# Kernel optimization log

Measured on AMD Instinct MI355X. Metric: run time of the kernel, lower is better.

Reference implementation:

```python
import jax, jax.numpy as jnp
import numpy as np

B, N, D = 4, 8192, 128
H = 4 * D  # exp_factor * features
EPS = 1e-5


def layer_norm(x):
    # fresh nn.LayerNorm each call -> weight=1, bias=0 (no learned affine)
    mu = jnp.mean(x, axis=-1, keepdims=True)
    var = jnp.var(x, axis=-1, keepdims=True)
    return (x - mu) * jax.lax.rsqrt(var + EPS)


def setup_inputs() -> dict:
    key = jax.random.key(0)
    ks = jax.random.split(key, 8)
    x = jax.random.normal(ks[0], (B, N, D), dtype=jnp.float32)
    adj = jax.random.uniform(ks[1], (N, N), dtype=jnp.float32)
    attn_mask = jnp.ones((1,), dtype=jnp.int32)  # unused (torch masked_fill result discarded)
    pad_mask = jnp.ones((1,), dtype=jnp.int32)   # unused
    # FFN params (torch Linear default init scale ~ 1/sqrt(fan_in))
    w1 = jax.random.normal(ks[2], (D, H), dtype=jnp.float32) / np.sqrt(D)
    b1 = jnp.zeros((H,), dtype=jnp.float32)
    w2 = jax.random.normal(ks[3], (H, D), dtype=jnp.float32) / np.sqrt(H)
    b2 = jnp.zeros((D,), dtype=jnp.float32)
    return {"x": x, "adj": adj, "attn_mask": attn_mask, "pad_mask": pad_mask,
            "w1": w1, "b1": b1, "w2": w2, "b2": b2, "dim": 128}


def reference(x, adj, attn_mask, pad_mask, w1, b1, w2, b2, dim):
    # Sublayer 0: x + InrAwaSA(LN(x))
    h = layer_norm(x)                               # [B,N,D]
    # adj is provided -> scores = dense adj, shared across batch.
    # NOTE: masks are no-ops in the source (masked_fill not in-place).
    prob = jax.nn.softmax(adj, axis=-1)             # [N,N]
    attn_out = jnp.einsum('nm,bmd->bnd', prob, h)   # [B,N,D]
    x1 = x + attn_out
    # Sublayer 1: x1 + FFN(LN(x1))
    h1 = layer_norm(x1)
    ffn = jnp.maximum(h1 @ w1 + b1, 0.0) @ w2 + b2
    return x1 + ffn
```

## Files before the change

kernel.cpp:

```cpp
#include <hip/hip_runtime.h>
#include <hip/hip_bf16.h>

typedef __attribute__((ext_vector_type(8))) short bh8;
typedef __attribute__((ext_vector_type(4))) float fx4;
typedef __attribute__((ext_vector_type(8))) int i32x8;
typedef __attribute__((ext_vector_type(4))) int i32x4;

typedef const __attribute__((address_space(1))) unsigned int* gas_p;
typedef __attribute__((address_space(3))) unsigned int* las_p;

#define MFMA(a, b, c) __builtin_amdgcn_mfma_f32_16x16x32_bf16((a), (b), (c), 0, 0, 0)
#define MFMAS(a, b, c) __builtin_amdgcn_mfma_scale_f32_16x16x128_f8f6f4( \
    (a), (b), (c), 0, 0, 0, 0x7f7f7f7f, 0, 0x7f7f7f7f)

__device__ __forceinline__ unsigned short f2bf(float f) {
  unsigned u = __builtin_bit_cast(unsigned, f);
  u += 0x7fff + ((u >> 16) & 1);
  return (unsigned short)(u >> 16);
}

__device__ __forceinline__ float bflo2f(unsigned u) { return __builtin_bit_cast(float, u << 16); }

__device__ __forceinline__ void gld16(const void* g, void* l) {
  __builtin_amdgcn_global_load_lds((gas_p)g, (las_p)l, 16, 0, 0);
}

__global__ __launch_bounds__(256) void transpose_weights(const float* __restrict__ w1,
                                                         const float* __restrict__ w2,
                                                         unsigned short* __restrict__ w1t,
                                                         unsigned short* __restrict__ w2t) {
  const int tgl = blockIdx.x * 256 + threadIdx.x;
  { const int h = tgl >> 7, d = tgl & 127; w1t[tgl] = f2bf(w1[d * 512 + h]); }
  { const int d = tgl >> 9, h = tgl & 511; w2t[tgl] = f2bf(w2[h * 128 + d]); }
}

__global__ __launch_bounds__(256) void ln1_transpose(const float* __restrict__ x,
                                                     unsigned char* __restrict__ ht) {
  const int t = threadIdx.x, lane = t & 63, w = t >> 6;
  const int mt = blockIdx.x, b = blockIdx.y;
  __shared__ unsigned short tile[128 * 64];
  const float* xb = x + ((size_t)b * 8192 + (size_t)mt * 64) * 128;
  for (int it = 0; it < 16; ++it) {
    const int r = w * 16 + it;
    const float2 v = *(const float2*)(xb + r * 128 + lane * 2);
    float s = v.x + v.y, s2 = v.x * v.x + v.y * v.y;
    #pragma unroll
    for (int o = 1; o < 64; o <<= 1) { s += __shfl_xor(s, o); s2 += __shfl_xor(s2, o); }
    const float mean = s * 0.0078125f;
    const float var = s2 * 0.0078125f - mean * mean;
    const float rstd = rsqrtf(var + 1e-5f);
    const int mc = r >> 3, ml = r & 7;
    const int d0 = lane * 2, d1 = d0 + 1;
    tile[d0 * 64 + ((mc ^ (d0 & 7)) << 3) + ml] = f2bf((v.x - mean) * rstd);
    tile[d1 * 64 + ((mc ^ (d1 & 7)) << 3) + ml] = f2bf((v.y - mean) * rstd);
  }
  __syncthreads();
  unsigned char* hb = ht + (size_t)b * 128 * 8192 + (size_t)mt * 64;
  #pragma unroll
  for (int i = 0; i < 4; ++i) {
    const int idx = i * 256 + t;
    const int d = idx >> 3, mc = idx & 7;
    const bh8 vv = *(const bh8*)(tile + d * 64 + ((mc ^ (d & 7)) << 3));
    int lo = 0, hi = 0;
    lo = __builtin_amdgcn_cvt_pk_fp8_f32(bflo2f((unsigned short)vv[0]),
                                         bflo2f((unsigned short)vv[1]), lo, false);
    lo = __builtin_amdgcn_cvt_pk_fp8_f32(bflo2f((unsigned short)vv[2]),
                                         bflo2f((unsigned short)vv[3]), lo, true);
    hi = __builtin_amdgcn_cvt_pk_fp8_f32(bflo2f((unsigned short)vv[4]),
                                         bflo2f((unsigned short)vv[5]), hi, false);
    hi = __builtin_amdgcn_cvt_pk_fp8_f32(bflo2f((unsigned short)vv[6]),
                                         bflo2f((unsigned short)vv[7]), hi, true);
    *(uint2*)(hb + (size_t)d * 8192 + mc * 8) = (uint2){(unsigned)lo, (unsigned)hi};
  }
}

__global__ __launch_bounds__(256) void softmax_rows(const float* __restrict__ adj,
                                                    unsigned char* __restrict__ prob) {
  const int t = threadIdx.x, lane = t & 63, w = t >> 6;
  const size_t r = blockIdx.x;
  __shared__ float red[4];
  const fx4* row = (const fx4*)(adj + r * 8192);
  fx4 v[8];
  float lsum = 0.f;
  #pragma unroll
  for (int i = 0; i < 8; ++i) {
    const fx4 a = row[i * 256 + t];
    fx4 e;
    e.x = __expf(a.x);
    e.y = __expf(a.y);
    e.z = __expf(a.z);
    e.w = __expf(a.w);
    v[i] = e;
    lsum += e.x + e.y + e.z + e.w;
  }
  #pragma unroll
  for (int o = 1; o < 64; o <<= 1) lsum += __shfl_xor(lsum, o);
  if (lane == 0) red[w] = lsum;
  __syncthreads();
  const float rinv = 4096.f / (red[0] + red[1] + red[2] + red[3]);
  unsigned* po = (unsigned*)(prob + r * 8192);
  #pragma unroll
  for (int i = 0; i < 8; ++i) {
    int pk = 0;
    pk = __builtin_amdgcn_cvt_pk_fp8_f32(v[i].x * rinv, v[i].y * rinv, pk, false);
    pk = __builtin_amdgcn_cvt_pk_fp8_f32(v[i].z * rinv, v[i].w * rinv, pk, true);
    po[i * 256 + t] = (unsigned)pk;
  }
}

#define PH_SYNC { __builtin_amdgcn_sched_barrier(0); __builtin_amdgcn_s_barrier(); \
                  __builtin_amdgcn_sched_barrier(0); \
                  asm volatile("s_waitcnt lgkmcnt(0)" ::: "memory"); \
                  __builtin_amdgcn_sched_barrier(0); __builtin_amdgcn_s_setprio(1); }
#define PH_END  { __builtin_amdgcn_s_setprio(0); __builtin_amdgcn_sched_barrier(0); \
                  __builtin_amdgcn_s_barrier(); __builtin_amdgcn_sched_barrier(0); }
#define PH_END_VM4 { __builtin_amdgcn_s_setprio(0); \
                  asm volatile("s_waitcnt vmcnt(4)" ::: "memory"); \
                  __builtin_amdgcn_sched_barrier(0); __builtin_amdgcn_s_barrier(); \
                  __builtin_amdgcn_sched_barrier(0); }

__global__ __launch_bounds__(512, 2) void attn_gemm(const unsigned char* __restrict__ prob,
                                                    const unsigned char* __restrict__ ht,
                                                    unsigned short* __restrict__ pbuf) {
  const int t = threadIdx.x, lane = t & 63, w = t >> 6;
  const int wm = w >> 2, wn = w & 3;
  const int mt = blockIdx.x, nt = blockIdx.y, z = blockIdx.z;
  const int kbase = z * 2048;

  __shared__ unsigned char Al[2][2][128 * 128];
  __shared__ unsigned char Bl[2][2][128 * 128];

  fx4 acc[8][4];
  #pragma unroll
  for (int i = 0; i < 8; ++i)
    #pragma unroll
    for (int j = 0; j < 4; ++j) acc[i][j] = (fx4){0.f, 0.f, 0.f, 0.f};

  i32x8 afr[4], bf0[2], bf1[2];

  auto stageA = [&](int buf, int half, int tau) {
    const unsigned char* root = prob + (size_t)(mt * 256 + half * 128) * 8192 + kbase + tau * 128;
    #pragma unroll
    for (int j = 0; j < 2; ++j) {
      const int idx = j * 512 + t;
      const int r = idx >> 3, g = idx & 7;
      gld16(root + (size_t)r * 8192 + ((g ^ (r & 7)) << 4), &Al[buf][half][idx * 16]);
    }
  };
  auto stageB = [&](int buf, int half, int tau) {
    const unsigned char* root = ht + (size_t)(nt * 256 + half * 128) * 8192 + kbase + tau * 128;
    #pragma unroll
    for (int j = 0; j < 2; ++j) {
      const int idx = j * 512 + t;
      const int r = idx >> 3, g = idx & 7;
      gld16(root + (size_t)r * 8192 + ((g ^ (r & 7)) << 4), &Bl[buf][half][idx * 16]);
    }
  };
  auto ldA = [&](int buf, int mh) {
    #pragma unroll
    for (int mf = 0; mf < 4; ++mf) {
      const int r = mh * 64 + mf * 16 + (lane & 15);
      const int gb = (lane >> 4) * 2;
      const unsigned char* base = &Al[buf][wm][r * 128];
      const i32x4 lo = *(const i32x4*)(base + ((gb ^ (r & 7)) << 4));
      const i32x4 hi = *(const i32x4*)(base + (((gb + 1) ^ (r & 7)) << 4));
      afr[mf] = (i32x8){lo.x, lo.y, lo.z, lo.w, hi.x, hi.y, hi.z, hi.w};
    }
  };
  auto ldB = [&](int buf, int nh, i32x8* dst) {
    #pragma unroll
    for (int nf = 0; nf < 2; ++nf) {
      const int c = (wn & 1) * 64 + nh * 32 + nf * 16 + (lane & 15);
      const int gb = (lane >> 4) * 2;
      const unsigned char* base = &Bl[buf][wn >> 1][c * 128];
      const i32x4 lo = *(const i32x4*)(base + ((gb ^ (c & 7)) << 4));
      const i32x4 hi = *(const i32x4*)(base + (((gb + 1) ^ (c & 7)) << 4));
      dst[nf] = (i32x8){lo.x, lo.y, lo.z, lo.w, hi.x, hi.y, hi.z, hi.w};
    }
  };
  auto mmq = [&](int mh, int nh, const i32x8* bfr) {
    #pragma unroll
    for (int mf = 0; mf < 4; ++mf)
      #pragma unroll
      for (int nf = 0; nf < 2; ++nf)
        acc[mh * 4 + mf][nh * 2 + nf] = MFMAS(afr[mf], bfr[nf], acc[mh * 4 + mf][nh * 2 + nf]);
  };

  stageA(0, 0, 0); stageA(0, 1, 0); stageB(0, 0, 0); stageB(0, 1, 0);
  stageB(1, 0, 1); stageB(1, 1, 1);
  asm volatile("s_waitcnt vmcnt(4)" ::: "memory");
  __builtin_amdgcn_sched_barrier(0);
  __builtin_amdgcn_s_barrier();
  __builtin_amdgcn_sched_barrier(0);

  for (int i = 0; i < 7; ++i) {
    const int t0 = 2 * i;
    ldA(0, 0); ldB(0, 0, bf0); stageA(1, 0, t0 + 1);
    PH_SYNC; mmq(0, 0, bf0); PH_END;
    ldB(0, 1, bf1); stageA(1, 1, t0 + 1);
    PH_SYNC; mmq(0, 1, bf1); PH_END;
    ldA(0, 1); stageB(0, 0, t0 + 2);
    PH_SYNC; mmq(1, 1, bf1); PH_END;
    stageB(0, 1, t0 + 2);
    PH_SYNC; mmq(1, 0, bf0); PH_END_VM4;
    ldA(1, 0); ldB(1, 0, bf0); stageA(0, 0, t0 + 2);
    PH_SYNC; mmq(0, 0, bf0); PH_END;
    ldB(1, 1, bf1); stageA(0, 1, t0 + 2);
    PH_SYNC; mmq(0, 1, bf1); PH_END;
    ldA(1, 1); stageB(1, 0, t0 + 3);
    PH_SYNC; mmq(1, 1, bf1); PH_END;
    stageB(1, 1, t0 + 3);
    PH_SYNC; mmq(1, 0, bf0); PH_END_VM4;
  }

  stageA(1, 0, 15); stageA(1, 1, 15);
  asm volatile("s_waitcnt vmcnt(0)" ::: "memory");
  __builtin_amdgcn_sched_barrier(0);
  __builtin_amdgcn_s_barrier();
  __builtin_amdgcn_sched_barrier(0);
  ldA(0, 0); ldB(0, 0, bf0); PH_SYNC; mmq(0, 0, bf0); PH_END;
  ldB(0, 1, bf1);            PH_SYNC; mmq(0, 1, bf1); PH_END;
  ldA(0, 1);                 PH_SYNC; mmq(1, 1, bf1); PH_END;
                             PH_SYNC; mmq(1, 0, bf0); PH_END;
  ldA(1, 0); ldB(1, 0, bf0); PH_SYNC; mmq(0, 0, bf0); PH_END;
  ldB(1, 1, bf1);            PH_SYNC; mmq(0, 1, bf1); PH_END;
  ldA(1, 1);                 PH_SYNC; mmq(1, 1, bf1); PH_END;
                             PH_SYNC; mmq(1, 0, bf0); PH_END;

  const float ds = 0.000244140625f;
  unsigned short* po = pbuf + (size_t)z * 8192 * 512;
  const int grow0 = mt * 256 + wm * 128;
  const int gcol0 = nt * 256 + (wn >> 1) * 128 + (wn & 1) * 64;
  #pragma unroll
  for (int mh = 0; mh < 2; ++mh)
    #pragma unroll
    for (int mf = 0; mf < 4; ++mf)
      #pragma unroll
      for (int nh = 0; nh < 2; ++nh)
        #pragma unroll
        for (int nf = 0; nf < 2; ++nf) {
          const int col = gcol0 + nh * 32 + nf * 16 + (lane & 15);
          #pragma unroll
          for (int q = 0; q < 4; ++q) {
            const int row = grow0 + mh * 64 + mf * 16 + (lane >> 4) * 4 + q;
            po[(size_t)row * 512 + col] = f2bf(acc[mh * 4 + mf][nh * 2 + nf][q] * ds);
          }
        }
}

#define SWZ16(ks, r) (((((ks) & 7) ^ ((r) & 7)) | ((ks) & 8)))
__global__ __launch_bounds__(512) void ln_ffn_kernel(const float* __restrict__ x,
                                                     const unsigned short* __restrict__ pbuf,
                                                     const unsigned short* __restrict__ w1t,
                                                     const unsigned short* __restrict__ w2t,
                                                     const float* __restrict__ b1,
                                                     const float* __restrict__ b2,
                                                     float* __restrict__ out) {
  const int t = threadIdx.x, lane = t & 63, w = t >> 6;
  const int wr = w >> 1, wc = w & 1;
  const int row0 = blockIdx.x * 128;
  __shared__ unsigned short As[128 * 128];
  __shared__ unsigned short W1c[128 * 128];
  __shared__ unsigned short W2c[128 * 128];
  __shared__ unsigned short Ts[128 * 128];

  auto stageW1 = [&](int hc) {
    #pragma unroll
    for (int i = 0; i < 4; ++i) {
      const int idx = i * 512 + t;
      const int row = idx >> 4, kc = idx & 15;
      const int kcs = (kc & 8) | ((kc & 7) ^ (row & 7));
      gld16(w1t + (size_t)(hc * 128 + row) * 128 + kcs * 8, W1c + (idx & ~63) * 8);
    }
  };
  auto stageW2 = [&](int hc) {
    #pragma unroll
    for (int i = 0; i < 4; ++i) {
      const int idx = i * 512 + t;
      const int row = idx >> 4, kc = idx & 15;
      const int kcs = (kc & 8) | ((kc & 7) ^ (row & 7));
      gld16(w2t + (size_t)row * 512 + hc * 128 + kcs * 8, W2c + (idx & ~63) * 8);
    }
  };

  stageW1(0); stageW2(0);

  const int r = t >> 2, q = t & 3, c0 = q * 32;
  const int rowg = row0 + r;
  const int bb = rowg >> 13, nn = rowg & 8191;
  float xv[32];
  {
    const float* xp = x + (size_t)rowg * 128 + c0;
    #pragma unroll
    for (int j = 0; j < 8; ++j) {
      const float4 v4 = *(const float4*)(xp + 4 * j);
      xv[4 * j] = v4.x; xv[4 * j + 1] = v4.y; xv[4 * j + 2] = v4.z; xv[4 * j + 3] = v4.w;
    }
    #pragma unroll
    for (int z = 0; z < 4; ++z) {
      const unsigned short* pp = pbuf + ((size_t)z * 8192 + nn) * 512 + bb * 128 + c0;
      #pragma unroll
      for (int j = 0; j < 4; ++j) {
        const bh8 pv = *(const bh8*)(pp + 8 * j);
        #pragma unroll
        for (int e = 0; e < 8; ++e) xv[8 * j + e] += bflo2f((unsigned short)pv[e]);
      }
    }
  }
  float s = 0.f, s2 = 0.f;
  #pragma unroll
  for (int j = 0; j < 32; ++j) { s += xv[j]; s2 += xv[j] * xv[j]; }
  s += __shfl_xor(s, 1); s2 += __shfl_xor(s2, 1);
  s += __shfl_xor(s, 2); s2 += __shfl_xor(s2, 2);
  const float mean = s * 0.0078125f;
  const float var = s2 * 0.0078125f - mean * mean;
  const float rstd = rsqrtf(var + 1e-5f);
  #pragma unroll
  for (int j = 0; j < 4; ++j) {
    const int g = q * 4 + j;
    bh8 pk;
    #pragma unroll
    for (int e = 0; e < 8; ++e) pk[e] = (short)f2bf((xv[8 * j + e] - mean) * rstd);
    *(bh8*)(As + r * 128 + SWZ16(g, r) * 8) = pk;
  }
  __syncthreads();

  fx4 accO[2][4];
  #pragma unroll
  for (int i = 0; i < 2; ++i)
    #pragma unroll
    for (int j = 0; j < 4; ++j) accO[i][j] = (fx4){0.f, 0.f, 0.f, 0.f};

  for (int hc = 0; hc < 4; ++hc) {
    if (hc > 0) stageW2(hc);
    fx4 accT[2][4];
    #pragma unroll
    for (int i = 0; i < 2; ++i)
      #pragma unroll
      for (int j = 0; j < 4; ++j) accT[i][j] = (fx4){0.f, 0.f, 0.f, 0.f};
    #pragma unroll
    for (int kk = 0; kk < 4; ++kk) {
      const int ks = kk * 4 + (lane >> 4);
      bh8 af[2], bfr[4];
      #pragma unroll
      for (int f = 0; f < 2; ++f) {
        const int ra = wr * 32 + f * 16 + (lane & 15);
        af[f] = *(const bh8*)(As + ra * 128 + SWZ16(ks, ra) * 8);
      }
      #pragma unroll
      for (int f = 0; f < 4; ++f) {
        const int rb = wc * 64 + f * 16 + (lane & 15);
        bfr[f] = *(const bh8*)(W1c + rb * 128 + SWZ16(ks, rb) * 8);
      }
      #pragma unroll
      for (int fm = 0; fm < 2; ++fm)
        #pragma unroll
        for (int fn = 0; fn < 4; ++fn) accT[fm][fn] = MFMA(af[fm], bfr[fn], accT[fm][fn]);
    }
    #pragma unroll
    for (int fm = 0; fm < 2; ++fm)
      #pragma unroll
      for (int fn = 0; fn < 4; ++fn) {
        const int col = wc * 64 + fn * 16 + (lane & 15);
        const float bv = b1[hc * 128 + col];
        const int c = col >> 3;
        #pragma unroll
        for (int qq = 0; qq < 4; ++qq) {
          const int row = wr * 32 + fm * 16 + (lane >> 4) * 4 + qq;
          float vv = accT[fm][fn][qq] + bv;
          vv = fmaxf(vv, 0.f);
          Ts[row * 128 + SWZ16(c, row) * 8 + (col & 7)] = f2bf(vv);
        }
      }
    __syncthreads();
    if (hc < 3) {
      stageW1(hc + 1);
    } else {
      float* dst = (r < 64) ? (float*)As + r * 128 + c0 : (float*)W1c + (r - 64) * 128 + c0;
      #pragma unroll
      for (int j = 0; j < 8; ++j)
        *(float4*)(dst + 4 * j) =
            (float4){xv[4 * j], xv[4 * j + 1], xv[4 * j + 2], xv[4 * j + 3]};
    }
    #pragma unroll
    for (int kk = 0; kk < 4; ++kk) {
      const int ks = kk * 4 + (lane >> 4);
      bh8 af[2], bfr[4];
      #pragma unroll
      for (int f = 0; f < 2; ++f) {
        const int ra = wr * 32 + f * 16 + (lane & 15);
        af[f] = *(const bh8*)(Ts + ra * 128 + SWZ16(ks, ra) * 8);
      }
      #pragma unroll
      for (int f = 0; f < 4; ++f) {
        const int rb = wc * 64 + f * 16 + (lane & 15);
        bfr[f] = *(const bh8*)(W2c + rb * 128 + SWZ16(ks, rb) * 8);
      }
      #pragma unroll
      for (int fm = 0; fm < 2; ++fm)
        #pragma unroll
        for (int fn = 0; fn < 4; ++fn) accO[fm][fn] = MFMA(af[fm], bfr[fn], accO[fm][fn]);
    }
    __syncthreads();
  }

  const float* x1a = (const float*)As;
  const float* x1b = (const float*)W1c;
  float* op = out + (size_t)row0 * 128;
  #pragma unroll
  for (int fm = 0; fm < 2; ++fm)
    #pragma unroll
    for (int fn = 0; fn < 4; ++fn) {
      const int col = wc * 64 + fn * 16 + (lane & 15);
      const float bv = b2[col];
      #pragma unroll
      for (int qq = 0; qq < 4; ++qq) {
        const int row = wr * 32 + fm * 16 + (lane >> 4) * 4 + qq;
        const float x1v = (row < 64) ? x1a[row * 128 + col] : x1b[(row - 64) * 128 + col];
        op[row * 128 + col] = x1v + accO[fm][fn][qq] + bv;
      }
    }
}

extern "C" void kernel_launch(void* const* d_in, const int* in_sizes, int n_in,
                              void* d_out, int out_size, void* d_ws, size_t ws_size,
                              hipStream_t stream) {
  const float* x   = (const float*)d_in[0];
  const float* adj = (const float*)d_in[1];
  const float* w1  = (const float*)d_in[4];
  const float* b1  = (const float*)d_in[5];
  const float* w2  = (const float*)d_in[6];
  const float* b2  = (const float*)d_in[7];
  float* out = (float*)d_out;

  char* p = (char*)d_ws;
  unsigned short* w1t  = (unsigned short*)p; p += (size_t)512 * 128 * 2;
  unsigned short* w2t  = (unsigned short*)p; p += (size_t)128 * 512 * 2;
  unsigned char*  ht   = (unsigned char*)p;  p += (size_t)4 * 128 * 8192;
  unsigned short* pbuf = (unsigned short*)p; p += (size_t)4 * 8192 * 512 * 2;
  unsigned char*  prob = (unsigned char*)p;  p += (size_t)8192 * 8192;

  transpose_weights<<<256, 256, 0, stream>>>(w1, w2, w1t, w2t);
  ln1_transpose<<<dim3(128, 4), 256, 0, stream>>>(x, ht);
  softmax_rows<<<8192, 256, 0, stream>>>(adj, prob);
  attn_gemm<<<dim3(32, 2, 4), 512, 0, stream>>>(prob, ht, pbuf);
  ln_ffn_kernel<<<256, 512, 0, stream>>>(x, pbuf, w1t, w2t, b1, b2, out);
}
```

Baseline: 157.6 us.

## Fuse softmax exponentiation into attention GEMM and defer normalization to LN-FFN

Removes the separate softmax kernel and its 64 MB fp8 probability buffer. The attention GEMM now reads fp32 adj directly, computes exp and converts to fp8 in registers, writes the A tile to LDS, and accumulates per-row partial denominators that are stored per K-split. The LN/FFN kernel sums the four partial denominators and scales the attention output by their reciprocal. The tile shape changes to 128 rows by all 512 columns with double-buffered B, so each block reads adj once. In exchange each block does exp work inside the GEMM loop, waits on vmcnt(0) each step, and stores unscaled exp values in fp8, which may reduce precision.

```diff
diff --git a/kernel.cpp b/kernel.cpp
--- a/kernel.cpp
+++ b/kernel.cpp
@@ -74,183 +74,142 @@
   }
 }
 
-__global__ __launch_bounds__(256) void softmax_rows(const float* __restrict__ adj,
-                                                    unsigned char* __restrict__ prob) {
-  const int t = threadIdx.x, lane = t & 63, w = t >> 6;
-  const size_t r = blockIdx.x;
-  __shared__ float red[4];
-  const fx4* row = (const fx4*)(adj + r * 8192);
-  fx4 v[8];
-  float lsum = 0.f;
-  #pragma unroll
-  for (int i = 0; i < 8; ++i) {
-    const fx4 a = row[i * 256 + t];
-    fx4 e;
-    e.x = __expf(a.x);
-    e.y = __expf(a.y);
-    e.z = __expf(a.z);
-    e.w = __expf(a.w);
-    v[i] = e;
-    lsum += e.x + e.y + e.z + e.w;
-  }
-  #pragma unroll
-  for (int o = 1; o < 64; o <<= 1) lsum += __shfl_xor(lsum, o);
-  if (lane == 0) red[w] = lsum;
-  __syncthreads();
-  const float rinv = 4096.f / (red[0] + red[1] + red[2] + red[3]);
-  unsigned* po = (unsigned*)(prob + r * 8192);
-  #pragma unroll
-  for (int i = 0; i < 8; ++i) {
-    int pk = 0;
-    pk = __builtin_amdgcn_cvt_pk_fp8_f32(v[i].x * rinv, v[i].y * rinv, pk, false);
-    pk = __builtin_amdgcn_cvt_pk_fp8_f32(v[i].z * rinv, v[i].w * rinv, pk, true);
-    po[i * 256 + t] = (unsigned)pk;
-  }
-}
-
 #define PH_SYNC { __builtin_amdgcn_sched_barrier(0); __builtin_amdgcn_s_barrier(); \
                   __builtin_amdgcn_sched_barrier(0); \
                   asm volatile("s_waitcnt lgkmcnt(0)" ::: "memory"); \
                   __builtin_amdgcn_sched_barrier(0); __builtin_amdgcn_s_setprio(1); }
 #define PH_END  { __builtin_amdgcn_s_setprio(0); __builtin_amdgcn_sched_barrier(0); \
                   __builtin_amdgcn_s_barrier(); __builtin_amdgcn_sched_barrier(0); }
-#define PH_END_VM4 { __builtin_amdgcn_s_setprio(0); \
-                  asm volatile("s_waitcnt vmcnt(4)" ::: "memory"); \
+#define PH_END_VM0 { __builtin_amdgcn_s_setprio(0); \
+                  asm volatile("s_waitcnt vmcnt(0)" ::: "memory"); \
                   __builtin_amdgcn_sched_barrier(0); __builtin_amdgcn_s_barrier(); \
                   __builtin_amdgcn_sched_barrier(0); }
 
-__global__ __launch_bounds__(512, 2) void attn_gemm(const unsigned char* __restrict__ prob,
-                                                    const unsigned char* __restrict__ ht,
-                                                    unsigned short* __restrict__ pbuf) {
-  const int t = threadIdx.x, lane = t & 63, w = t >> 6;
+__global__ __launch_bounds__(512, 2) void fused_attn(const float* __restrict__ adj,
+                                                     const unsigned char* __restrict__ ht,
+                                                     unsigned short* __restrict__ pbuf,
+                                                     float* __restrict__ sden) {
+  const int tid = threadIdx.x, lane = tid & 63, w = tid >> 6;
   const int wm = w >> 2, wn = w & 3;
-  const int mt = blockIdx.x, nt = blockIdx.y, z = blockIdx.z;
+  const int mt = blockIdx.x, z = blockIdx.y;
   const int kbase = z * 2048;
 
-  __shared__ unsigned char Al[2][2][128 * 128];
-  __shared__ unsigned char Bl[2][2][128 * 128];
-
-  fx4 acc[8][4];
-  #pragma unroll
-  for (int i = 0; i < 8; ++i)
-    #pragma unroll
-    for (int j = 0; j < 4; ++j) acc[i][j] = (fx4){0.f, 0.f, 0.f, 0.f};
-
-  i32x8 afr[4], bf0[2], bf1[2];
-
-  auto stageA = [&](int buf, int half, int tau) {
-    const unsigned char* root = prob + (size_t)(mt * 256 + half * 128) * 8192 + kbase + tau * 128;
-    #pragma unroll
-    for (int j = 0; j < 2; ++j) {
-      const int idx = j * 512 + t;
-      const int r = idx >> 3, g = idx & 7;
-      gld16(root + (size_t)r * 8192 + ((g ^ (r & 7)) << 4), &Al[buf][half][idx * 16]);
-    }
-  };
-  auto stageB = [&](int buf, int half, int tau) {
-    const unsigned char* root = ht + (size_t)(nt * 256 + half * 128) * 8192 + kbase + tau * 128;
-    #pragma unroll
-    for (int j = 0; j < 2; ++j) {
-      const int idx = j * 512 + t;
-      const int r = idx >> 3, g = idx & 7;
-      gld16(root + (size_t)r * 8192 + ((g ^ (r & 7)) << 4), &Bl[buf][half][idx * 16]);
-    }
-  };
-  auto ldA = [&](int buf, int mh) {
+  __shared__ unsigned char Al[128 * 128];
+  __shared__ unsigned char Bl[2][512 * 128];
+
+  fx4 acc[4][8];
+  #pragma unroll
+  for (int i = 0; i < 4; ++i)
+    #pragma unroll
+    for (int j = 0; j < 8; ++j) acc[i][j] = (fx4){0.f, 0.f, 0.f, 0.f};
+
+  i32x8 afr[4];
+
+  const int ar = tid >> 2, aq = tid & 3;
+  const float* aroot = adj + (size_t)(mt * 128 + ar) * 8192 + kbase;
+  float sacc = 0.f;
+  float4 a4[8];
+  unsigned pk[8];
+
+  auto issueAdj = [&](int tau) {
+    #pragma unroll
+    for (int j = 0; j < 8; ++j)
+      a4[j] = *(const float4*)(aroot + tau * 128 + j * 16 + aq * 4);
+  };
+  auto expCvt = [&]() {
+    #pragma unroll
+    for (int j = 0; j < 8; ++j) {
+      const float e0 = __expf(a4[j].x), e1 = __expf(a4[j].y);
+      const float e2 = __expf(a4[j].z), e3 = __expf(a4[j].w);
+      sacc += (e0 + e1) + (e2 + e3);
+      int d = 0;
+      d = __builtin_amdgcn_cvt_pk_fp8_f32(e0, e1, d, false);
+      d = __builtin_amdgcn_cvt_pk_fp8_f32(e2, e3, d, true);
+      pk[j] = (unsigned)d;
+    }
+  };
+  auto writeA = [&]() {
+    #pragma unroll
+    for (int j = 0; j < 8; ++j)
+      *(unsigned*)&Al[ar * 128 + ((j ^ (ar & 7)) << 4) + aq * 4] = pk[j];
+  };
+  auto stageB2 = [&](unsigned char* dst, int pp, int tau) {
+    #pragma unroll
+    for (int k = 0; k < 2; ++k) {
+      const int cc = pp * 2 + k;
+      const int row = cc * 64 + (tid >> 3), g = tid & 7;
+      gld16(ht + (size_t)row * 8192 + kbase + tau * 128 + ((g ^ (row & 7)) << 4),
+            dst + cc * 8192 + tid * 16);
+    }
+  };
+  auto ldAall = [&]() {
     #pragma unroll
     for (int mf = 0; mf < 4; ++mf) {
-      const int r = mh * 64 + mf * 16 + (lane & 15);
+      const int rr = wm * 64 + mf * 16 + (lane & 15);
       const int gb = (lane >> 4) * 2;
-      const unsigned char* base = &Al[buf][wm][r * 128];
-      const i32x4 lo = *(const i32x4*)(base + ((gb ^ (r & 7)) << 4));
-      const i32x4 hi = *(const i32x4*)(base + (((gb + 1) ^ (r & 7)) << 4));
+      const unsigned char* base = &Al[rr * 128];
+      const i32x4 lo = *(const i32x4*)(base + ((gb ^ (rr & 7)) << 4));
+      const i32x4 hi = *(const i32x4*)(base + (((gb + 1) ^ (rr & 7)) << 4));
       afr[mf] = (i32x8){lo.x, lo.y, lo.z, lo.w, hi.x, hi.y, hi.z, hi.w};
     }
   };
-  auto ldB = [&](int buf, int nh, i32x8* dst) {
-    #pragma unroll
-    for (int nf = 0; nf < 2; ++nf) {
-      const int c = (wn & 1) * 64 + nh * 32 + nf * 16 + (lane & 15);
-      const int gb = (lane >> 4) * 2;
-      const unsigned char* base = &Bl[buf][wn >> 1][c * 128];
-      const i32x4 lo = *(const i32x4*)(base + ((gb ^ (c & 7)) << 4));
-      const i32x4 hi = *(const i32x4*)(base + (((gb + 1) ^ (c & 7)) << 4));
-      dst[nf] = (i32x8){lo.x, lo.y, lo.z, lo.w, hi.x, hi.y, hi.z, hi.w};
-    }
-  };
-  auto mmq = [&](int mh, int nh, const i32x8* bfr) {
-    #pragma unroll
-    for (int mf = 0; mf < 4; ++mf)
-      #pragma unroll
-      for (int nf = 0; nf < 2; ++nf)
-        acc[mh * 4 + mf][nh * 2 + nf] = MFMAS(afr[mf], bfr[nf], acc[mh * 4 + mf][nh * 2 + nf]);
-  };
-
-  stageA(0, 0, 0); stageA(0, 1, 0); stageB(0, 0, 0); stageB(0, 1, 0);
-  stageB(1, 0, 1); stageB(1, 1, 1);
-  asm volatile("s_waitcnt vmcnt(4)" ::: "memory");
+
+  issueAdj(0);
+  #pragma unroll
+  for (int pp = 0; pp < 4; ++pp) stageB2(Bl[0], pp, 0);
+  expCvt();
+  writeA();
+  asm volatile("s_waitcnt lgkmcnt(0) vmcnt(0)" ::: "memory");
   __builtin_amdgcn_sched_barrier(0);
   __builtin_amdgcn_s_barrier();
   __builtin_amdgcn_sched_barrier(0);
 
-  for (int i = 0; i < 7; ++i) {
-    const int t0 = 2 * i;
-    ldA(0, 0); ldB(0, 0, bf0); stageA(1, 0, t0 + 1);
-    PH_SYNC; mmq(0, 0, bf0); PH_END;
-    ldB(0, 1, bf1); stageA(1, 1, t0 + 1);
-    PH_SYNC; mmq(0, 1, bf1); PH_END;
-    ldA(0, 1); stageB(0, 0, t0 + 2);
-    PH_SYNC; mmq(1, 1, bf1); PH_END;
-    stageB(0, 1, t0 + 2);
-    PH_SYNC; mmq(1, 0, bf0); PH_END_VM4;
-    ldA(1, 0); ldB(1, 0, bf0); stageA(0, 0, t0 + 2);
-    PH_SYNC; mmq(0, 0, bf0); PH_END;
-    ldB(1, 1, bf1); stageA(0, 1, t0 + 2);
-    PH_SYNC; mmq(0, 1, bf1); PH_END;
-    ldA(1, 1); stageB(1, 0, t0 + 3);
-    PH_SYNC; mmq(1, 1, bf1); PH_END;
-    stageB(1, 1, t0 + 3);
-    PH_SYNC; mmq(1, 0, bf0); PH_END_VM4;
-  }
-
-  stageA(1, 0, 15); stageA(1, 1, 15);
-  asm volatile("s_waitcnt vmcnt(0)" ::: "memory");
-  __builtin_amdgcn_sched_barrier(0);
-  __builtin_amdgcn_s_barrier();
-  __builtin_amdgcn_sched_barrier(0);
-  ldA(0, 0); ldB(0, 0, bf0); PH_SYNC; mmq(0, 0, bf0); PH_END;
-  ldB(0, 1, bf1);            PH_SYNC; mmq(0, 1, bf1); PH_END;
-  ldA(0, 1);                 PH_SYNC; mmq(1, 1, bf1); PH_END;
-                             PH_SYNC; mmq(1, 0, bf0); PH_END;
-  ldA(1, 0); ldB(1, 0, bf0); PH_SYNC; mmq(0, 0, bf0); PH_END;
-  ldB(1, 1, bf1);            PH_SYNC; mmq(0, 1, bf1); PH_END;
-  ldA(1, 1);                 PH_SYNC; mmq(1, 1, bf1); PH_END;
-                             PH_SYNC; mmq(1, 0, bf0); PH_END;
-
-  const float ds = 0.000244140625f;
+  for (int tt = 0; tt < 16; ++tt) {
+    const unsigned char* Bcur = Bl[tt & 1];
+    unsigned char* Bnxt = Bl[(tt + 1) & 1];
+    const bool more = (tt < 15);
+    #pragma unroll
+    for (int p = 0; p < 8; ++p) {
+      const int c = wn * 128 + p * 16 + (lane & 15);
+      const int gb = (lane >> 4) * 2;
+      const unsigned char* cb = &Bcur[c * 128];
+      const i32x4 blo = *(const i32x4*)(cb + ((gb ^ (c & 7)) << 4));
+      const i32x4 bhi = *(const i32x4*)(cb + (((gb + 1) ^ (c & 7)) << 4));
+      const i32x8 bfr = (i32x8){blo.x, blo.y, blo.z, blo.w, bhi.x, bhi.y, bhi.z, bhi.w};
+      if (p == 0) { ldAall(); if (more) issueAdj(tt + 1); }
+      if (p < 4 && more) stageB2(Bnxt, p, tt + 1);
+      if (p == 5 && more) expCvt();
+      if (p == 6 && more) writeA();
+      PH_SYNC;
+      #pragma unroll
+      for (int mf = 0; mf < 4; ++mf)
+        acc[mf][p] = MFMAS(afr[mf], bfr, acc[mf][p]);
+      if (p == 7) { PH_END_VM0; } else { PH_END; }
+    }
+  }
+
+  sacc += __shfl_xor(sacc, 1);
+  sacc += __shfl_xor(sacc, 2);
+  if (aq == 0) sden[(size_t)z * 8192 + mt * 128 + ar] = sacc;
+
   unsigned short* po = pbuf + (size_t)z * 8192 * 512;
-  const int grow0 = mt * 256 + wm * 128;
-  const int gcol0 = nt * 256 + (wn >> 1) * 128 + (wn & 1) * 64;
-  #pragma unroll
-  for (int mh = 0; mh < 2; ++mh)
-    #pragma unroll
-    for (int mf = 0; mf < 4; ++mf)
-      #pragma unroll
-      for (int nh = 0; nh < 2; ++nh)
-        #pragma unroll
-        for (int nf = 0; nf < 2; ++nf) {
-          const int col = gcol0 + nh * 32 + nf * 16 + (lane & 15);
-          #pragma unroll
-          for (int q = 0; q < 4; ++q) {
-            const int row = grow0 + mh * 64 + mf * 16 + (lane >> 4) * 4 + q;
-            po[(size_t)row * 512 + col] = f2bf(acc[mh * 4 + mf][nh * 2 + nf][q] * ds);
-          }
-        }
+  #pragma unroll
+  for (int mf = 0; mf < 4; ++mf)
+    #pragma unroll
+    for (int nf = 0; nf < 8; ++nf) {
+      const int col = wn * 128 + nf * 16 + (lane & 15);
+      #pragma unroll
+      for (int q = 0; q < 4; ++q) {
+        const int row = mt * 128 + wm * 64 + mf * 16 + (lane >> 4) * 4 + q;
+        po[(size_t)row * 512 + col] = f2bf(acc[mf][nf][q]);
+      }
+    }
 }
 
 #define SWZ16(ks, r) (((((ks) & 7) ^ ((r) & 7)) | ((ks) & 8)))
 __global__ __launch_bounds__(512) void ln_ffn_kernel(const float* __restrict__ x,
                                                      const unsigned short* __restrict__ pbuf,
+                                                     const float* __restrict__ sden,
                                                      const unsigned short* __restrict__ w1t,
                                                      const unsigned short* __restrict__ w2t,
                                                      const float* __restrict__ b1,
@@ -290,6 +249,8 @@
   const int bb = rowg >> 13, nn = rowg & 8191;
   float xv[32];
   {
+    const float den = sden[nn] + sden[8192 + nn] + sden[16384 + nn] + sden[24576 + nn];
+    const float rinv = 1.f / den;
     const float* xp = x + (size_t)rowg * 128 + c0;
     #pragma unroll
     for (int j = 0; j < 8; ++j) {
@@ -303,7 +264,7 @@
       for (int j = 0; j < 4; ++j) {
         const bh8 pv = *(const bh8*)(pp + 8 * j);
         #pragma unroll
-        for (int e = 0; e < 8; ++e) xv[8 * j + e] += bflo2f((unsigned short)pv[e]);
+        for (int e = 0; e < 8; ++e) xv[8 * j + e] += bflo2f((unsigned short)pv[e]) * rinv;
       }
     }
   }
@@ -438,11 +399,10 @@
   unsigned short* w2t  = (unsigned short*)p; p += (size_t)128 * 512 * 2;
   unsigned char*  ht   = (unsigned char*)p;  p += (size_t)4 * 128 * 8192;
   unsigned short* pbuf = (unsigned short*)p; p += (size_t)4 * 8192 * 512 * 2;
-  unsigned char*  prob = (unsigned char*)p;  p += (size_t)8192 * 8192;
+  float*          sden = (float*)p;          p += (size_t)4 * 8192 * 4;
 
   transpose_weights<<<256, 256, 0, stream>>>(w1, w2, w1t, w2t);
   ln1_transpose<<<dim3(128, 4), 256, 0, stream>>>(x, ht);
-  softmax_rows<<<8192, 256, 0, stream>>>(adj, prob);
-  attn_gemm<<<dim3(32, 2, 4), 512, 0, stream>>>(prob, ht, pbuf);
-  ln_ffn_kernel<<<256, 512, 0, stream>>>(x, pbuf, w1t, w2t, b1, b2, out);
-}
+  fused_attn<<<dim3(64, 4), 512, 0, stream>>>(adj, ht, pbuf, sden);
+  ln_ffn_kernel<<<256, 512, 0, stream>>>(x, pbuf, sden, w1t, w2t, b1, b2, out);
+}
```

New measurement: 151.5 us. 3.9% less time.
